# Kernel optimization log

Measured on AMD Instinct MI355X. Metric: run time of the kernel, lower is better.

## Reference

```python
import jax, jax.numpy as jnp
import numpy as np

N = 50000
E = 400000  # bidirectional: second half is reverse of first half
D = 128
T = 3
EPS = 1e-09


def apply_lambda(x, log_dt, log_lambda_real, lambda_imag, one_minus=False):
    # lambda_complex = exp((-exp(log_lambda_real) + 1j*lambda_imag) * dt)
    dt = jnp.exp(log_dt)
    mag = jnp.exp(-jnp.exp(log_lambda_real) * dt)          # |lambda| [D//2]
    mag = jnp.where(one_minus, 1.0 - mag, mag)
    phase = lambda_imag * dt                                # angle (cos/sin are wrap-invariant)
    c, s = jnp.cos(phase), jnp.sin(phase)
    xp = x.reshape(x.shape[:-1] + (-1, 2))                  # [..., D//2, 2]
    xr = (c * xp[..., 0] - s * xp[..., 1]) * mag
    xi = (s * xp[..., 0] + c * xp[..., 1]) * mag
    return jnp.stack((xr, xi), axis=-1).reshape(x.shape)


def setup_inputs() -> dict:
    key = jax.random.key(0)
    kx, ke1, ke2, k1, k2, k3, k4 = jax.random.split(key, 7)
    x = jax.random.normal(kx, (N, D), dtype=jnp.float32)
    a = jax.random.randint(ke1, (E // 2,), 0, N)
    b = jax.random.randint(ke2, (E // 2,), 0, N)
    edge_index = jnp.stack([jnp.concatenate([a, b]), jnp.concatenate([b, a])], axis=0)
    hidden = D + D
    scale1 = 1.0 / np.sqrt(D)
    scale2 = 1.0 / np.sqrt(hidden)
    return {
        "x": x,
        "edge_index": edge_index,
        "log_dt": jnp.asarray(np.log(0.1), dtype=jnp.float32),
        "log_lambda_real": jnp.full((D // 2,), np.log(0.5), dtype=jnp.float32),
        "lambda_imag": jnp.arange(D // 2, dtype=jnp.float32) * np.pi,
        "W1": jax.random.uniform(k1, (D, hidden), jnp.float32, -scale1, scale1),
        "W2": jax.random.uniform(k2, (D, hidden), jnp.float32, -scale1, scale1),
        "Wp": jax.random.uniform(k3, (hidden, D), jnp.float32, -scale2, scale2),
        "bp": jax.random.uniform(k4, (D,), jnp.float32, -scale2, scale2),
    }


def reference(x, edge_index, log_dt, log_lambda_real, lambda_imag, W1, W2, Wp, bp):
    x_in = x  # dim_in == dim_out -> residual from pre-MLP input
    # MLP: silu(x W1) * (x W2) -> proj
    h = jax.nn.silu(x @ W1) * (x @ W2)
    x = h @ Wp + bp

    lam = lambda v, om=False: apply_lambda(v, log_dt, log_lambda_real, lambda_imag, om)
    src, dst = edge_index[0], edge_index[1]

    deg = jax.ops.segment_sum(jnp.ones((E,), x.dtype), src, num_segments=N)  # [N]
    M = x[src]                                                              # [E, D]
    m = jax.ops.segment_sum(M, dst, num_segments=N)                         # [N, D]

    for _ in range(T):
        M_ji = jnp.concatenate((M[E // 2:], M[:E // 2]), axis=0)            # reverse-edge message
        x_e = x[src]
        deg_e = deg[src][:, None]
        M = jnp.where(deg_e == 1,
                      x_e,
                      lam(x_e, True) + lam(m[src] - M_ji) / (deg_e - 1 + EPS))
        m = jax.ops.segment_sum(M, dst, num_segments=N)

    out = jnp.where(deg[:, None] == 0, x, lam(x, True) + lam(m) / (deg[:, None] + EPS))
    out = jax.nn.relu(out)  # dropout p=0 (eval)
    return x_in + out
```

## Files before the change

kernel.cpp:

```cpp
#include <hip/hip_runtime.h>

#define EPSF 1e-9f

typedef __bf16 bf16x8 __attribute__((ext_vector_type(8)));
typedef float  f32x4  __attribute__((ext_vector_type(4)));
typedef unsigned short ushort_t;
typedef unsigned int uint_t;
typedef ushort_t us8 __attribute__((ext_vector_type(8)));

__device__ __forceinline__ float2 cmul(float cr, float ci, float2 v) {
    return make_float2(cr * v.x - ci * v.y, ci * v.x + cr * v.y);
}

__device__ __forceinline__ ushort_t f2bf(float f) {
    unsigned int u = __float_as_uint(f);
    u += 0x7FFFu + ((u >> 16) & 1u);
    return (ushort_t)(u >> 16);
}

__device__ __forceinline__ float2 bfu2(uint_t u) {
    return make_float2(__uint_as_float(u << 16), __uint_as_float(u & 0xFFFF0000u));
}
__device__ __forceinline__ uint_t packbf(float2 v) {
    return ((uint_t)f2bf(v.y) << 16) | (uint_t)f2bf(v.x);
}

__global__ void k_lamtab(const float* __restrict__ ldt, const float* __restrict__ llr,
                         const float* __restrict__ lim, float* __restrict__ tab) {
    int p = threadIdx.x;
    if (p >= 64) return;
    float dt  = expf(ldt[0]);
    float mag = expf(-expf(llr[p]) * dt);
    float ph  = lim[p] * dt;
    float c = cosf(ph), s = sinf(ph);
    float m2 = mag * mag, m3 = m2 * mag;
    float c2 = c * c - s * s, s2 = 2.f * c * s;
    float c3 = c2 * c - s2 * s, s3 = s2 * c + c2 * s;
    tab[p]        = c * mag;          tab[64 + p]  = s * mag;
    tab[128 + p]  = c * (1.f - mag);  tab[192 + p] = s * (1.f - mag);
    tab[256 + p]  = c2 * m2;          tab[320 + p] = s2 * m2;
    tab[384 + p]  = c3 * m3;          tab[448 + p] = s3 * m3;
}

__global__ void k_prepw(const float* __restrict__ w, ushort_t* __restrict__ wb,
                        int ncols, int nsteps, int total) {
    int tid = blockIdx.x * blockDim.x + threadIdx.x;
    if (tid >= total) return;
    int l  = tid & 63;
    int s  = (tid >> 6) % nsteps;
    int nt = tid / (64 * nsteps);
    int col = nt * 16 + (l & 15);
    int kb  = s * 32 + (l >> 4) * 8;
    us8 d;
#pragma unroll
    for (int j = 0; j < 8; ++j) d[j] = f2bf(w[(size_t)(kb + j) * ncols + col]);
    *(us8*)(wb + (size_t)tid * 8) = d;
}

__global__ void __launch_bounds__(256)
k_mlpf(const float* __restrict__ x, const ushort_t* __restrict__ wb1,
       const ushort_t* __restrict__ wb2, const ushort_t* __restrict__ wpb,
       const float* __restrict__ bp, ushort_t* __restrict__ xpb, int Mt) {
    __shared__ ushort_t hs[2][4096];
    const int wid = threadIdx.x >> 6, l = threadIdx.x & 63;
    const int mt0 = blockIdx.x * 2;
    const bool has1 = (mt0 + 1) < Mt;
    const int llo = l & 15, lhi = l >> 4;

    bf16x8 af[2][4];
#pragma unroll
    for (int m = 0; m < 2; ++m) {
        int mt = (m == 1 && !has1) ? mt0 : (mt0 + m);
        const float* xr = x + (size_t)(mt * 16 + llo) * 128 + lhi * 8;
#pragma unroll
        for (int s = 0; s < 4; ++s) {
            float4 v0 = *(const float4*)(xr + s * 32);
            float4 v1 = *(const float4*)(xr + s * 32 + 4);
            us8 d;
            d[0] = f2bf(v0.x); d[1] = f2bf(v0.y); d[2] = f2bf(v0.z); d[3] = f2bf(v0.w);
            d[4] = f2bf(v1.x); d[5] = f2bf(v1.y); d[6] = f2bf(v1.z); d[7] = f2bf(v1.w);
            af[m][s] = *(bf16x8*)&d;
        }
    }

    const bf16x8* B1 = (const bf16x8*)wb1;
    const bf16x8* B2 = (const bf16x8*)wb2;
    const bf16x8* BP = (const bf16x8*)wpb;
    const f32x4 zero = {0.f, 0.f, 0.f, 0.f};

#pragma unroll
    for (int j = 0; j < 4; ++j) {
        int nt = wid * 4 + j;
        bf16x8 b1[4], b2[4];
#pragma unroll
        for (int s = 0; s < 4; ++s) {
            b1[s] = B1[(nt * 4 + s) * 64 + l];
            b2[s] = B2[(nt * 4 + s) * 64 + l];
        }
#pragma unroll
        for (int m = 0; m < 2; ++m) {
            f32x4 a1 = zero, a2 = zero;
#pragma unroll
            for (int s = 0; s < 4; ++s) {
                a1 = __builtin_amdgcn_mfma_f32_16x16x32_bf16(af[m][s], b1[s], a1, 0, 0, 0);
                a2 = __builtin_amdgcn_mfma_f32_16x16x32_bf16(af[m][s], b2[s], a2, 0, 0, 0);
            }
#pragma unroll
            for (int i = 0; i < 4; ++i) {
                float g = a1[i];
                float hv = (g / (1.f + __expf(-g))) * a2[i];
                int r = 4 * lhi + i;
                int byte = (r << 9) + ((nt * 16 + llo) << 1);
                byte ^= (r & 7) << 4;
                hs[m][byte >> 1] = f2bf(hv);
            }
        }
    }
    __syncthreads();

#pragma unroll
    for (int j = 0; j < 2; ++j) {
        int nt3 = wid * 2 + j;
        f32x4 acc0 = zero, acc1 = zero;
#pragma unroll
        for (int sg = 0; sg < 8; ++sg) {
            bf16x8 bw = BP[(nt3 * 8 + sg) * 64 + l];
            int byte = (llo << 9) + (sg << 6) + (lhi << 4);
            byte ^= (llo & 7) << 4;
            bf16x8 h0 = *(const bf16x8*)((const char*)hs[0] + byte);
            acc0 = __builtin_amdgcn_mfma_f32_16x16x32_bf16(h0, bw, acc0, 0, 0, 0);
            bf16x8 h1 = *(const bf16x8*)((const char*)hs[1] + byte);
            acc1 = __builtin_amdgcn_mfma_f32_16x16x32_bf16(h1, bw, acc1, 0, 0, 0);
        }
        float bpv = bp[nt3 * 16 + llo];
        {
            const int row0 = mt0 * 16;
#pragma unroll
            for (int i = 0; i < 4; ++i) {
                int r = row0 + 4 * lhi + i;
                xpb[(size_t)r * 128 + nt3 * 16 + llo] = f2bf(acc0[i] + bpv);
            }
        }
        if (has1) {
            const int row0 = (mt0 + 1) * 16;
#pragma unroll
            for (int i = 0; i < 4; ++i) {
                int r = row0 + 4 * lhi + i;
                xpb[(size_t)r * 128 + nt3 * 16 + llo] = f2bf(acc1[i] + bpv);
            }
        }
    }
}

__global__ void k_hist(const int* __restrict__ ei, int E, int* __restrict__ cnt) {
    int e = blockIdx.x * blockDim.x + threadIdx.x;
    if (e < E) atomicAdd(&cnt[ei[E + e]], 1);
}

__global__ void __launch_bounds__(256)
k_scanA(const int* __restrict__ cnt, int N, int* __restrict__ bsum) {
    __shared__ int s[256];
    int t = threadIdx.x;
    int i = blockIdx.x * 256 + t;
    int v = (i < N) ? cnt[i] : 0;
    s[t] = v;
    __syncthreads();
#pragma unroll
    for (int d = 128; d > 0; d >>= 1) {
        if (t < d) s[t] += s[t + d];
        __syncthreads();
    }
    if (t == 0) bsum[blockIdx.x] = s[0];
}

__global__ void __launch_bounds__(1024)
k_scanB(const int* __restrict__ bsum, int NB, int* __restrict__ bpre,
        int* __restrict__ offN) {
    __shared__ int s[1024];
    int t = threadIdx.x;
    int v = (t < NB) ? bsum[t] : 0;
    s[t] = v;
    __syncthreads();
    for (int d = 1; d < 1024; d <<= 1) {
        int u = (t >= d) ? s[t - d] : 0;
        __syncthreads();
        s[t] += u;
        __syncthreads();
    }
    if (t < NB) bpre[t] = s[t] - v;
    if (t == NB - 1) *offN = s[t];
}

__global__ void __launch_bounds__(256)
k_scanC(const int* __restrict__ cnt, int N, const int* __restrict__ bpre,
        int* __restrict__ off, int* __restrict__ cursor, float* __restrict__ bv) {
    __shared__ int s[256];
    int t = threadIdx.x;
    int i = blockIdx.x * 256 + t;
    int v = (i < N) ? cnt[i] : 0;
    s[t] = v;
    __syncthreads();
    for (int d = 1; d < 256; d <<= 1) {
        int u = (t >= d) ? s[t - d] : 0;
        __syncthreads();
        s[t] += u;
        __syncthreads();
    }
    if (i < N) {
        int excl = bpre[blockIdx.x] + s[t] - v;
        off[i] = excl;
        cursor[i] = excl;
        bv[i] = (v > 1) ? (-1.f / ((float)v - 1.f + EPSF)) : 0.f;
    }
}

__global__ void k_fill(const int* __restrict__ ei, int E,
                       int* __restrict__ cursor, int* __restrict__ csr) {
    int e = blockIdx.x * blockDim.x + threadIdx.x;
    if (e < E) {
        int s = ei[e], d = ei[E + e];
        int p = atomicAdd(&cursor[d], 1);
        csr[p] = s;
    }
}

__global__ void __launch_bounds__(256)
k_passA(const ushort_t* __restrict__ xpb, const float* __restrict__ bv,
        const int* __restrict__ off, const int* __restrict__ csr,
        const float* __restrict__ tab, ushort_t* __restrict__ Xbb,
        ushort_t* __restrict__ a1b, int N) {
    int tid = blockIdx.x * blockDim.x + threadIdx.x;
    int v = tid >> 6, l = tid & 63;
    if (v >= N) return;
    int beg = off[v], end = off[v + 1];
    float2 m0 = make_float2(0.f, 0.f), xb = make_float2(0.f, 0.f);
    const uint_t* tb = (const uint_t*)xpb;
    int k = beg;
    for (; k + 1 < end; k += 2) {
        int s0 = csr[k], s1 = csr[k + 1];
        uint_t u0 = tb[(size_t)s0 * 64 + l];
        uint_t u1 = tb[(size_t)s1 * 64 + l];
        float b0 = bv[s0], b1 = bv[s1];
        float2 t0 = bfu2(u0), t1v = bfu2(u1);
        m0.x += t0.x + t1v.x;        m0.y += t0.y + t1v.y;
        xb.x += b0 * t0.x + b1 * t1v.x;
        xb.y += b0 * t0.y + b1 * t1v.y;
    }
    if (k < end) {
        int s0 = csr[k];
        float2 t0 = bfu2(tb[(size_t)s0 * 64 + l]);
        float b0 = bv[s0];
        m0.x += t0.x; m0.y += t0.y;
        xb.x += b0 * t0.x; xb.y += b0 * t0.y;
    }
    ((uint_t*)Xbb)[(size_t)v * 64 + l] = packbf(xb);
    float2 xv = bfu2(tb[(size_t)v * 64 + l]);
    int dg = end - beg;
    float L1r = tab[l], L1i = tab[64 + l], O1r = tab[128 + l], O1i = tab[192 + l];
    float Q = 1.f / ((float)dg - 1.f + EPSF);
    float2 t1 = cmul(O1r, O1i, xv);
    float2 t2 = cmul(L1r, L1i, m0);
    float2 a = make_float2(t1.x + Q * t2.x, t1.y + Q * t2.y);
    if (dg == 1) a = xv;
    ((uint_t*)a1b)[(size_t)v * 64 + l] = packbf(a);
}

__global__ void __launch_bounds__(256)
k_passB(const ushort_t* __restrict__ xpb, const ushort_t* __restrict__ a1b,
        const float* __restrict__ bv, const int* __restrict__ off,
        const int* __restrict__ csr, const float* __restrict__ tab,
        ushort_t* __restrict__ ab1b, float* __restrict__ Bv, float* __restrict__ B2v,
        ushort_t* __restrict__ a2b, int N) {
    int tid = blockIdx.x * blockDim.x + threadIdx.x;
    int v = tid >> 6, l = tid & 63;
    if (v >= N) return;
    int beg = off[v], end = off[v + 1];
    float2 A1 = make_float2(0.f, 0.f), ab = make_float2(0.f, 0.f);
    float Bs = 0.f, B2s = 0.f;
    const uint_t* tb = (const uint_t*)a1b;
    int k = beg;
    for (; k + 1 < end; k += 2) {
        int s0 = csr[k], s1 = csr[k + 1];
        uint_t u0 = tb[(size_t)s0 * 64 + l];
        uint_t u1 = tb[(size_t)s1 * 64 + l];
        float b0 = bv[s0], b1 = bv[s1];
        float2 t0 = bfu2(u0), t1v = bfu2(u1);
        A1.x += t0.x + t1v.x;  A1.y += t0.y + t1v.y;
        ab.x += b0 * t0.x + b1 * t1v.x;
        ab.y += b0 * t0.y + b1 * t1v.y;
        Bs += b0 + b1; B2s += b0 * b0 + b1 * b1;
    }
    if (k < end) {
        int s0 = csr[k];
        float2 t0 = bfu2(tb[(size_t)s0 * 64 + l]);
        float b0 = bv[s0];
        A1.x += t0.x; A1.y += t0.y;
        ab.x += b0 * t0.x; ab.y += b0 * t0.y;
        Bs += b0; B2s += b0 * b0;
    }
    ((uint_t*)ab1b)[(size_t)v * 64 + l] = packbf(ab);
    if (l == 0) { Bv[v] = Bs; B2v[v] = B2s; }
    float2 xv = bfu2(((const uint_t*)xpb)[(size_t)v * 64 + l]);
    int dg = end - beg;
    float L1r = tab[l], L1i = tab[64 + l], O1r = tab[128 + l], O1i = tab[192 + l];
    float2 lx = cmul(L1r, L1i, xv);
    float2 m1 = make_float2(A1.x + Bs * lx.x, A1.y + Bs * lx.y);
    float Q = 1.f / ((float)dg - 1.f + EPSF);
    float2 t1 = cmul(O1r, O1i, xv);
    float2 lm = cmul(L1r, L1i, m1);
    float2 a = make_float2(t1.x + Q * lm.x, t1.y + Q * lm.y);
    if (dg == 1) a = xv;
    ((uint_t*)a2b)[(size_t)v * 64 + l] = packbf(a);
}

__global__ void __launch_bounds__(256)
k_passC(const ushort_t* __restrict__ xpb, const ushort_t* __restrict__ a2b,
        const ushort_t* __restrict__ a1b, const ushort_t* __restrict__ Xbb,
        const float* __restrict__ bv, const float* __restrict__ Bv,
        const int* __restrict__ off, const int* __restrict__ csr,
        const float* __restrict__ tab, ushort_t* __restrict__ a3b, int N) {
    int tid = blockIdx.x * blockDim.x + threadIdx.x;
    int v = tid >> 6, l = tid & 63;
    if (v >= N) return;
    int beg = off[v], end = off[v + 1];
    float2 A2 = make_float2(0.f, 0.f);
    const uint_t* tb = (const uint_t*)a2b;
    int k = beg;
    for (; k + 1 < end; k += 2) {
        int s0 = csr[k], s1 = csr[k + 1];
        float2 t0 = bfu2(tb[(size_t)s0 * 64 + l]);
        float2 t1v = bfu2(tb[(size_t)s1 * 64 + l]);
        A2.x += t0.x + t1v.x; A2.y += t0.y + t1v.y;
    }
    if (k < end) {
        float2 t0 = bfu2(tb[(size_t)csr[k] * 64 + l]);
        A2.x += t0.x; A2.y += t0.y;
    }
    float2 xv  = bfu2(((const uint_t*)xpb)[(size_t)v * 64 + l]);
    float2 a1v = bfu2(((const uint_t*)a1b)[(size_t)v * 64 + l]);
    float2 Xbv = bfu2(((const uint_t*)Xbb)[(size_t)v * 64 + l]);
    int dg = end - beg;
    float Bs = Bv[v], bs = bv[v];
    float L1r = tab[l], L1i = tab[64 + l], O1r = tab[128 + l], O1i = tab[192 + l];
    float L2r = tab[256 + l], L2i = tab[320 + l];
    float2 la1 = cmul(L1r, L1i, a1v);
    float2 lxb = cmul(L2r, L2i, Xbv);
    float2 m2 = make_float2(A2.x + Bs * la1.x + bs * lxb.x,
                            A2.y + Bs * la1.y + bs * lxb.y);
    float Q = 1.f / ((float)dg - 1.f + EPSF);
    float2 t1 = cmul(O1r, O1i, xv);
    float2 lm = cmul(L1r, L1i, m2);
    float2 a = make_float2(t1.x + Q * lm.x, t1.y + Q * lm.y);
    if (dg == 1) a = xv;
    ((uint_t*)a3b)[(size_t)v * 64 + l] = packbf(a);
}

__global__ void __launch_bounds__(256)
k_passD(const float* __restrict__ xin, const ushort_t* __restrict__ xpb,
        const ushort_t* __restrict__ a3b, const ushort_t* __restrict__ a2b,
        const ushort_t* __restrict__ ab1b, const float* __restrict__ bv,
        const float* __restrict__ Bv, const float* __restrict__ B2v,
        const int* __restrict__ off, const int* __restrict__ csr,
        const float* __restrict__ tab, float* __restrict__ out, int N) {
    int tid = blockIdx.x * blockDim.x + threadIdx.x;
    int v = tid >> 6, l = tid & 63;
    if (v >= N) return;
    int beg = off[v], end = off[v + 1];
    float2 A3 = make_float2(0.f, 0.f);
    const uint_t* tb = (const uint_t*)a3b;
    int k = beg;
    for (; k + 1 < end; k += 2) {
        int s0 = csr[k], s1 = csr[k + 1];
        float2 t0 = bfu2(tb[(size_t)s0 * 64 + l]);
        float2 t1v = bfu2(tb[(size_t)s1 * 64 + l]);
        A3.x += t0.x + t1v.x; A3.y += t0.y + t1v.y;
    }
    if (k < end) {
        float2 t0 = bfu2(tb[(size_t)csr[k] * 64 + l]);
        A3.x += t0.x; A3.y += t0.y;
    }
    size_t o = (size_t)v * 128 + 2 * l;
    float2 xv  = bfu2(((const uint_t*)xpb)[(size_t)v * 64 + l]);
    float2 a2v = bfu2(((const uint_t*)a2b)[(size_t)v * 64 + l]);
    float2 Abv = bfu2(((const uint_t*)ab1b)[(size_t)v * 64 + l]);
    int dg = end - beg;
    float Bs = Bv[v], bs = bv[v], B2s = B2v[v];
    float L1r = tab[l], L1i = tab[64 + l], O1r = tab[128 + l], O1i = tab[192 + l];
    float L2r = tab[256 + l], L2i = tab[320 + l];
    float L3r = tab[384 + l], L3i = tab[448 + l];
    float2 la2 = cmul(L1r, L1i, a2v);
    float2 lab = cmul(L2r, L2i, Abv);
    float2 lx3 = cmul(L3r, L3i, xv);
    float bB2 = bs * B2s;
    float2 m3 = make_float2(A3.x + Bs * la2.x + bs * lab.x + bB2 * lx3.x,
                            A3.y + Bs * la2.y + bs * lab.y + bB2 * lx3.y);
    float2 g;
    if (dg == 0) {
        g = xv;
    } else {
        float inv = 1.f / ((float)dg + EPSF);
        float2 t1 = cmul(O1r, O1i, xv);
        float2 lm = cmul(L1r, L1i, m3);
        g = make_float2(t1.x + lm.x * inv, t1.y + lm.y * inv);
    }
    float2 xi = *(const float2*)&xin[o];
    float2 res = make_float2(xi.x + fmaxf(g.x, 0.f), xi.y + fmaxf(g.y, 0.f));
    *(float2*)&out[o] = res;
}

extern "C" void kernel_launch(void* const* d_in, const int* in_sizes, int n_in,
                              void* d_out, int out_size, void* d_ws, size_t ws_size,
                              hipStream_t stream) {
    const float* x   = (const float*)d_in[0];
    const int*   ei  = (const int*)d_in[1];
    const float* ldt = (const float*)d_in[2];
    const float* llr = (const float*)d_in[3];
    const float* lim = (const float*)d_in[4];
    const float* W1  = (const float*)d_in[5];
    const float* W2  = (const float*)d_in[6];
    const float* Wp  = (const float*)d_in[7];
    const float* bp  = (const float*)d_in[8];
    float* out = (float*)d_out;

    const int N = in_sizes[0] / 128;
    const int E = in_sizes[1] / 2;
    const size_t nd = (size_t)N * 128;
    const int Mt = (N + 15) / 16;
    const int Mt2 = (Mt + 1) / 2;
    const int NB = (N + 255) / 256;

    ushort_t* xpb  = (ushort_t*)d_ws;
    ushort_t* a1b  = xpb + nd;
    ushort_t* a2b  = a1b + nd;
    ushort_t* a3b  = a2b + nd;
    ushort_t* Xbb  = a3b + nd;
    ushort_t* ab1b = Xbb + nd;

    int*   cnt    = (int*)(ab1b + nd);
    int*   off    = cnt + N;
    int*   cursor = off + N + 4;
    float* bv     = (float*)(cursor + N);
    float* Bv     = bv + N;
    float* B2v    = Bv + N;
    float* tab    = B2v + N;
    int*   bsum   = (int*)(tab + 512);
    int*   bpre   = bsum + NB;
    int*   csr    = bpre + NB;
    ushort_t* wb1 = (ushort_t*)(csr + E);
    ushort_t* wb2 = wb1 + 32768;
    ushort_t* wpb = wb2 + 32768;

    const int nodeBlocks = (int)(((size_t)N * 64 + 255) / 256);
    const int eBlocks    = (E + 255) / 256;

    hipMemsetAsync(cnt, 0, (size_t)N * sizeof(int), stream);
    k_lamtab<<<1, 64, 0, stream>>>(ldt, llr, lim, tab);

    k_prepw<<<16, 256, 0, stream>>>(W1, wb1, 256, 4, 16 * 4 * 64);
    k_prepw<<<16, 256, 0, stream>>>(W2, wb2, 256, 4, 16 * 4 * 64);
    k_prepw<<<16, 256, 0, stream>>>(Wp, wpb, 128, 8, 8 * 8 * 64);
    k_mlpf<<<Mt2, 256, 0, stream>>>(x, wb1, wb2, wpb, bp, xpb, Mt);

    k_hist<<<eBlocks, 256, 0, stream>>>(ei, E, cnt);
    k_scanA<<<NB, 256, 0, stream>>>(cnt, N, bsum);
    k_scanB<<<1, 1024, 0, stream>>>(bsum, NB, bpre, &off[N]);
    k_scanC<<<NB, 256, 0, stream>>>(cnt, N, bpre, off, cursor, bv);
    k_fill<<<eBlocks, 256, 0, stream>>>(ei, E, cursor, csr);

    k_passA<<<nodeBlocks, 256, 0, stream>>>(xpb, bv, off, csr, tab, Xbb, a1b, N);
    k_passB<<<nodeBlocks, 256, 0, stream>>>(xpb, a1b, bv, off, csr, tab, ab1b, Bv, B2v, a2b, N);
    k_passC<<<nodeBlocks, 256, 0, stream>>>(xpb, a2b, a1b, Xbb, bv, Bv, off, csr, tab, a3b, N);
    k_passD<<<nodeBlocks, 256, 0, stream>>>(x, xpb, a3b, a2b, ab1b, bv, Bv, B2v, off, csr, tab, out, N);
}
```

Baseline: 236.9 us.

## Split node feature arrays into four column quarters for cache-local gathers

Node feature buffers move from row-major [N,128] bf16 to four column-quarter planes [4][N,32]. Each gather pass now runs on a 2D grid where blockIdx.y picks the quarter and 16 lanes handle one node's 64-byte slice. The aim is to shrink the working set each group of blocks touches so the random neighbor gathers hit L2 more often. In exchange, the csr, offset and bv reads are repeated four times, each gather fetches only 64 bytes, and the MLP writes become strided.

```diff
diff --git a/kernel.cpp b/kernel.cpp
--- a/kernel.cpp
+++ b/kernel.cpp
@@ -60,7 +60,7 @@
 __global__ void __launch_bounds__(256)
 k_mlpf(const float* __restrict__ x, const ushort_t* __restrict__ wb1,
        const ushort_t* __restrict__ wb2, const ushort_t* __restrict__ wpb,
-       const float* __restrict__ bp, ushort_t* __restrict__ xpb, int Mt) {
+       const float* __restrict__ bp, ushort_t* __restrict__ xpb, int Mt, int Nn) {
     __shared__ ushort_t hs[2][4096];
     const int wid = threadIdx.x >> 6, l = threadIdx.x & 63;
     const int mt0 = blockIdx.x * 2;
@@ -118,6 +118,7 @@
     }
     __syncthreads();
 
+    const size_t qsN = (size_t)Nn * 32;
 #pragma unroll
     for (int j = 0; j < 2; ++j) {
         int nt3 = wid * 2 + j;
@@ -133,12 +134,15 @@
             acc1 = __builtin_amdgcn_mfma_f32_16x16x32_bf16(h1, bw, acc1, 0, 0, 0);
         }
         float bpv = bp[nt3 * 16 + llo];
+        int col = nt3 * 16 + llo;
+        int q = col >> 5, wc = col & 31;
+        size_t qb = (size_t)q * qsN;
         {
             const int row0 = mt0 * 16;
 #pragma unroll
             for (int i = 0; i < 4; ++i) {
                 int r = row0 + 4 * lhi + i;
-                xpb[(size_t)r * 128 + nt3 * 16 + llo] = f2bf(acc0[i] + bpv);
+                if (r < Nn) xpb[qb + (size_t)r * 32 + wc] = f2bf(acc0[i] + bpv);
             }
         }
         if (has1) {
@@ -146,7 +150,7 @@
 #pragma unroll
             for (int i = 0; i < 4; ++i) {
                 int r = row0 + 4 * lhi + i;
-                xpb[(size_t)r * 128 + nt3 * 16 + llo] = f2bf(acc1[i] + bpv);
+                if (r < Nn) xpb[qb + (size_t)r * 32 + wc] = f2bf(acc1[i] + bpv);
             }
         }
     }
@@ -224,22 +228,26 @@
     }
 }
 
+
 __global__ void __launch_bounds__(256)
 k_passA(const ushort_t* __restrict__ xpb, const float* __restrict__ bv,
         const int* __restrict__ off, const int* __restrict__ csr,
         const float* __restrict__ tab, ushort_t* __restrict__ Xbb,
         ushort_t* __restrict__ a1b, int N) {
-    int tid = blockIdx.x * blockDim.x + threadIdx.x;
-    int v = tid >> 6, l = tid & 63;
+    int t = threadIdx.x;
+    int v = blockIdx.x * 16 + (t >> 4);
+    int c = t & 15;
+    int q = blockIdx.y;
     if (v >= N) return;
+    const size_t qs = (size_t)N * 16;
+    const uint_t* tb = (const uint_t*)xpb + (size_t)q * qs;
     int beg = off[v], end = off[v + 1];
     float2 m0 = make_float2(0.f, 0.f), xb = make_float2(0.f, 0.f);
-    const uint_t* tb = (const uint_t*)xpb;
     int k = beg;
     for (; k + 1 < end; k += 2) {
         int s0 = csr[k], s1 = csr[k + 1];
-        uint_t u0 = tb[(size_t)s0 * 64 + l];
-        uint_t u1 = tb[(size_t)s1 * 64 + l];
+        uint_t u0 = tb[(size_t)s0 * 16 + c];
+        uint_t u1 = tb[(size_t)s1 * 16 + c];
         float b0 = bv[s0], b1 = bv[s1];
         float2 t0 = bfu2(u0), t1v = bfu2(u1);
         m0.x += t0.x + t1v.x;        m0.y += t0.y + t1v.y;
@@ -248,21 +256,22 @@
     }
     if (k < end) {
         int s0 = csr[k];
-        float2 t0 = bfu2(tb[(size_t)s0 * 64 + l]);
+        float2 t0 = bfu2(tb[(size_t)s0 * 16 + c]);
         float b0 = bv[s0];
         m0.x += t0.x; m0.y += t0.y;
         xb.x += b0 * t0.x; xb.y += b0 * t0.y;
     }
-    ((uint_t*)Xbb)[(size_t)v * 64 + l] = packbf(xb);
-    float2 xv = bfu2(tb[(size_t)v * 64 + l]);
+    ((uint_t*)Xbb + (size_t)q * qs)[(size_t)v * 16 + c] = packbf(xb);
+    float2 xv = bfu2(tb[(size_t)v * 16 + c]);
     int dg = end - beg;
-    float L1r = tab[l], L1i = tab[64 + l], O1r = tab[128 + l], O1i = tab[192 + l];
+    int p = q * 16 + c;
+    float L1r = tab[p], L1i = tab[64 + p], O1r = tab[128 + p], O1i = tab[192 + p];
     float Q = 1.f / ((float)dg - 1.f + EPSF);
     float2 t1 = cmul(O1r, O1i, xv);
     float2 t2 = cmul(L1r, L1i, m0);
     float2 a = make_float2(t1.x + Q * t2.x, t1.y + Q * t2.y);
     if (dg == 1) a = xv;
-    ((uint_t*)a1b)[(size_t)v * 64 + l] = packbf(a);
+    ((uint_t*)a1b + (size_t)q * qs)[(size_t)v * 16 + c] = packbf(a);
 }
 
 __global__ void __launch_bounds__(256)
@@ -271,18 +280,21 @@
         const int* __restrict__ csr, const float* __restrict__ tab,
         ushort_t* __restrict__ ab1b, float* __restrict__ Bv, float* __restrict__ B2v,
         ushort_t* __restrict__ a2b, int N) {
-    int tid = blockIdx.x * blockDim.x + threadIdx.x;
-    int v = tid >> 6, l = tid & 63;
+    int t = threadIdx.x;
+    int v = blockIdx.x * 16 + (t >> 4);
+    int c = t & 15;
+    int q = blockIdx.y;
     if (v >= N) return;
+    const size_t qs = (size_t)N * 16;
+    const uint_t* tb = (const uint_t*)a1b + (size_t)q * qs;
     int beg = off[v], end = off[v + 1];
     float2 A1 = make_float2(0.f, 0.f), ab = make_float2(0.f, 0.f);
     float Bs = 0.f, B2s = 0.f;
-    const uint_t* tb = (const uint_t*)a1b;
     int k = beg;
     for (; k + 1 < end; k += 2) {
         int s0 = csr[k], s1 = csr[k + 1];
-        uint_t u0 = tb[(size_t)s0 * 64 + l];
-        uint_t u1 = tb[(size_t)s1 * 64 + l];
+        uint_t u0 = tb[(size_t)s0 * 16 + c];
+        uint_t u1 = tb[(size_t)s1 * 16 + c];
         float b0 = bv[s0], b1 = bv[s1];
         float2 t0 = bfu2(u0), t1v = bfu2(u1);
         A1.x += t0.x + t1v.x;  A1.y += t0.y + t1v.y;
@@ -292,17 +304,18 @@
     }
     if (k < end) {
         int s0 = csr[k];
-        float2 t0 = bfu2(tb[(size_t)s0 * 64 + l]);
+        float2 t0 = bfu2(tb[(size_t)s0 * 16 + c]);
         float b0 = bv[s0];
         A1.x += t0.x; A1.y += t0.y;
         ab.x += b0 * t0.x; ab.y += b0 * t0.y;
         Bs += b0; B2s += b0 * b0;
     }
-    ((uint_t*)ab1b)[(size_t)v * 64 + l] = packbf(ab);
-    if (l == 0) { Bv[v] = Bs; B2v[v] = B2s; }
-    float2 xv = bfu2(((const uint_t*)xpb)[(size_t)v * 64 + l]);
+    ((uint_t*)ab1b + (size_t)q * qs)[(size_t)v * 16 + c] = packbf(ab);
+    if (q == 0 && c == 0) { Bv[v] = Bs; B2v[v] = B2s; }
+    float2 xv = bfu2(((const uint_t*)xpb + (size_t)q * qs)[(size_t)v * 16 + c]);
     int dg = end - beg;
-    float L1r = tab[l], L1i = tab[64 + l], O1r = tab[128 + l], O1i = tab[192 + l];
+    int p = q * 16 + c;
+    float L1r = tab[p], L1i = tab[64 + p], O1r = tab[128 + p], O1i = tab[192 + p];
     float2 lx = cmul(L1r, L1i, xv);
     float2 m1 = make_float2(A1.x + Bs * lx.x, A1.y + Bs * lx.y);
     float Q = 1.f / ((float)dg - 1.f + EPSF);
@@ -310,7 +323,7 @@
     float2 lm = cmul(L1r, L1i, m1);
     float2 a = make_float2(t1.x + Q * lm.x, t1.y + Q * lm.y);
     if (dg == 1) a = xv;
-    ((uint_t*)a2b)[(size_t)v * 64 + l] = packbf(a);
+    ((uint_t*)a2b + (size_t)q * qs)[(size_t)v * 16 + c] = packbf(a);
 }
 
 __global__ void __launch_bounds__(256)
@@ -319,30 +332,35 @@
         const float* __restrict__ bv, const float* __restrict__ Bv,
         const int* __restrict__ off, const int* __restrict__ csr,
         const float* __restrict__ tab, ushort_t* __restrict__ a3b, int N) {
-    int tid = blockIdx.x * blockDim.x + threadIdx.x;
-    int v = tid >> 6, l = tid & 63;
+    int t = threadIdx.x;
+    int v = blockIdx.x * 16 + (t >> 4);
+    int c = t & 15;
+    int q = blockIdx.y;
     if (v >= N) return;
+    const size_t qs = (size_t)N * 16;
+    const uint_t* tb = (const uint_t*)a2b + (size_t)q * qs;
     int beg = off[v], end = off[v + 1];
     float2 A2 = make_float2(0.f, 0.f);
-    const uint_t* tb = (const uint_t*)a2b;
     int k = beg;
     for (; k + 1 < end; k += 2) {
         int s0 = csr[k], s1 = csr[k + 1];
-        float2 t0 = bfu2(tb[(size_t)s0 * 64 + l]);
-        float2 t1v = bfu2(tb[(size_t)s1 * 64 + l]);
+        float2 t0 = bfu2(tb[(size_t)s0 * 16 + c]);
+        float2 t1v = bfu2(tb[(size_t)s1 * 16 + c]);
         A2.x += t0.x + t1v.x; A2.y += t0.y + t1v.y;
     }
     if (k < end) {
-        float2 t0 = bfu2(tb[(size_t)csr[k] * 64 + l]);
+        float2 t0 = bfu2(tb[(size_t)csr[k] * 16 + c]);
         A2.x += t0.x; A2.y += t0.y;
     }
-    float2 xv  = bfu2(((const uint_t*)xpb)[(size_t)v * 64 + l]);
-    float2 a1v = bfu2(((const uint_t*)a1b)[(size_t)v * 64 + l]);
-    float2 Xbv = bfu2(((const uint_t*)Xbb)[(size_t)v * 64 + l]);
+    size_t vo = (size_t)v * 16 + c;
+    float2 xv  = bfu2(((const uint_t*)xpb + (size_t)q * qs)[vo]);
+    float2 a1v = bfu2(((const uint_t*)a1b + (size_t)q * qs)[vo]);
+    float2 Xbv = bfu2(((const uint_t*)Xbb + (size_t)q * qs)[vo]);
     int dg = end - beg;
     float Bs = Bv[v], bs = bv[v];
-    float L1r = tab[l], L1i = tab[64 + l], O1r = tab[128 + l], O1i = tab[192 + l];
-    float L2r = tab[256 + l], L2i = tab[320 + l];
+    int p = q * 16 + c;
+    float L1r = tab[p], L1i = tab[64 + p], O1r = tab[128 + p], O1i = tab[192 + p];
+    float L2r = tab[256 + p], L2i = tab[320 + p];
     float2 la1 = cmul(L1r, L1i, a1v);
     float2 lxb = cmul(L2r, L2i, Xbv);
     float2 m2 = make_float2(A2.x + Bs * la1.x + bs * lxb.x,
@@ -352,7 +370,7 @@
     float2 lm = cmul(L1r, L1i, m2);
     float2 a = make_float2(t1.x + Q * lm.x, t1.y + Q * lm.y);
     if (dg == 1) a = xv;
-    ((uint_t*)a3b)[(size_t)v * 64 + l] = packbf(a);
+    ((uint_t*)a3b + (size_t)q * qs)[vo] = packbf(a);
 }
 
 __global__ void __launch_bounds__(256)
@@ -362,32 +380,36 @@
         const float* __restrict__ Bv, const float* __restrict__ B2v,
         const int* __restrict__ off, const int* __restrict__ csr,
         const float* __restrict__ tab, float* __restrict__ out, int N) {
-    int tid = blockIdx.x * blockDim.x + threadIdx.x;
-    int v = tid >> 6, l = tid & 63;
+    int t = threadIdx.x;
+    int v = blockIdx.x * 16 + (t >> 4);
+    int c = t & 15;
+    int q = blockIdx.y;
     if (v >= N) return;
+    const size_t qs = (size_t)N * 16;
+    const uint_t* tb = (const uint_t*)a3b + (size_t)q * qs;
     int beg = off[v], end = off[v + 1];
     float2 A3 = make_float2(0.f, 0.f);
-    const uint_t* tb = (const uint_t*)a3b;
     int k = beg;
     for (; k + 1 < end; k += 2) {
         int s0 = csr[k], s1 = csr[k + 1];
-        float2 t0 = bfu2(tb[(size_t)s0 * 64 + l]);
-        float2 t1v = bfu2(tb[(size_t)s1 * 64 + l]);
+        float2 t0 = bfu2(tb[(size_t)s0 * 16 + c]);
+        float2 t1v = bfu2(tb[(size_t)s1 * 16 + c]);
         A3.x += t0.x + t1v.x; A3.y += t0.y + t1v.y;
     }
     if (k < end) {
-        float2 t0 = bfu2(tb[(size_t)csr[k] * 64 + l]);
+        float2 t0 = bfu2(tb[(size_t)csr[k] * 16 + c]);
         A3.x += t0.x; A3.y += t0.y;
     }
-    size_t o = (size_t)v * 128 + 2 * l;
-    float2 xv  = bfu2(((const uint_t*)xpb)[(size_t)v * 64 + l]);
-    float2 a2v = bfu2(((const uint_t*)a2b)[(size_t)v * 64 + l]);
-    float2 Abv = bfu2(((const uint_t*)ab1b)[(size_t)v * 64 + l]);
+    size_t vo = (size_t)v * 16 + c;
+    float2 xv  = bfu2(((const uint_t*)xpb + (size_t)q * qs)[vo]);
+    float2 a2v = bfu2(((const uint_t*)a2b + (size_t)q * qs)[vo]);
+    float2 Abv = bfu2(((const uint_t*)ab1b + (size_t)q * qs)[vo]);
     int dg = end - beg;
     float Bs = Bv[v], bs = bv[v], B2s = B2v[v];
-    float L1r = tab[l], L1i = tab[64 + l], O1r = tab[128 + l], O1i = tab[192 + l];
-    float L2r = tab[256 + l], L2i = tab[320 + l];
-    float L3r = tab[384 + l], L3i = tab[448 + l];
+    int p = q * 16 + c;
+    float L1r = tab[p], L1i = tab[64 + p], O1r = tab[128 + p], O1i = tab[192 + p];
+    float L2r = tab[256 + p], L2i = tab[320 + p];
+    float L3r = tab[384 + p], L3i = tab[448 + p];
     float2 la2 = cmul(L1r, L1i, a2v);
     float2 lab = cmul(L2r, L2i, Abv);
     float2 lx3 = cmul(L3r, L3i, xv);
@@ -403,6 +425,7 @@
         float2 lm = cmul(L1r, L1i, m3);
         g = make_float2(t1.x + lm.x * inv, t1.y + lm.y * inv);
     }
+    size_t o = (size_t)v * 128 + 2 * p;
     float2 xi = *(const float2*)&xin[o];
     float2 res = make_float2(xi.x + fmaxf(g.x, 0.f), xi.y + fmaxf(g.y, 0.f));
     *(float2*)&out[o] = res;
@@ -450,8 +473,8 @@
     ushort_t* wb2 = wb1 + 32768;
     ushort_t* wpb = wb2 + 32768;
 
-    const int nodeBlocks = (int)(((size_t)N * 64 + 255) / 256);
-    const int eBlocks    = (E + 255) / 256;
+    const int eBlocks = (E + 255) / 256;
+    dim3 gp((N + 15) / 16, 4);
 
     hipMemsetAsync(cnt, 0, (size_t)N * sizeof(int), stream);
     k_lamtab<<<1, 64, 0, stream>>>(ldt, llr, lim, tab);
@@ -459,7 +482,7 @@
     k_prepw<<<16, 256, 0, stream>>>(W1, wb1, 256, 4, 16 * 4 * 64);
     k_prepw<<<16, 256, 0, stream>>>(W2, wb2, 256, 4, 16 * 4 * 64);
     k_prepw<<<16, 256, 0, stream>>>(Wp, wpb, 128, 8, 8 * 8 * 64);
-    k_mlpf<<<Mt2, 256, 0, stream>>>(x, wb1, wb2, wpb, bp, xpb, Mt);
+    k_mlpf<<<Mt2, 256, 0, stream>>>(x, wb1, wb2, wpb, bp, xpb, Mt, N);
 
     k_hist<<<eBlocks, 256, 0, stream>>>(ei, E, cnt);
     k_scanA<<<NB, 256, 0, stream>>>(cnt, N, bsum);
@@ -467,8 +490,8 @@
     k_scanC<<<NB, 256, 0, stream>>>(cnt, N, bpre, off, cursor, bv);
     k_fill<<<eBlocks, 256, 0, stream>>>(ei, E, cursor, csr);
 
-    k_passA<<<nodeBlocks, 256, 0, stream>>>(xpb, bv, off, csr, tab, Xbb, a1b, N);
-    k_passB<<<nodeBlocks, 256, 0, stream>>>(xpb, a1b, bv, off, csr, tab, ab1b, Bv, B2v, a2b, N);
-    k_passC<<<nodeBlocks, 256, 0, stream>>>(xpb, a2b, a1b, Xbb, bv, Bv, off, csr, tab, a3b, N);
-    k_passD<<<nodeBlocks, 256, 0, stream>>>(x, xpb, a3b, a2b, ab1b, bv, Bv, B2v, off, csr, tab, out, N);
-}
+    k_passA<<<gp, 256, 0, stream>>>(xpb, bv, off, csr, tab, Xbb, a1b, N);
+    k_passB<<<gp, 256, 0, stream>>>(xpb, a1b, bv, off, csr, tab, ab1b, Bv, B2v, a2b, N);
+    k_passC<<<gp, 256, 0, stream>>>(xpb, a2b, a1b, Xbb, bv, Bv, off, csr, tab, a3b, N);
+    k_passD<<<gp, 256, 0, stream>>>(x, xpb, a3b, a2b, ab1b, bv, Bv, B2v, off, csr, tab, out, N);
+}
```

After: 269.8 us. +13.9%, slower.
